# Kernel tuning notes

Hardware: AMD Instinct MI355X
Metric: run time of the kernel (lower is better)

The kernel has to match this reference:

```python
import jax, jax.numpy as jnp
import numpy as np

B, H, C, D = 32, 12, 512, 768
M = 8            # mentions per entity
EMB, BLK = 768, 8
NCLS, NER = 97, 6
OFFSET = 1       # [CLS] offset as in get_hrt


def setup_inputs() -> dict:
    key = jax.random.key(0)
    ks = jax.random.split(key, 10)
    sequence_output = jax.random.normal(ks[0], (B, C, D), jnp.float32)
    attention = jax.random.uniform(ks[1], (B, H, C, C), jnp.float32)
    ner_tags = jax.random.uniform(ks[2], (B, 2, NER), jnp.float32)
    W_head = jax.random.normal(ks[3], (EMB, 2 * D + NER), jnp.float32) * 0.02
    b_head = jnp.zeros((EMB,), jnp.float32)
    W_tail = jax.random.normal(ks[4], (EMB, 2 * D + NER), jnp.float32) * 0.02
    b_tail = jnp.zeros((EMB,), jnp.float32)
    W_bil = jax.random.normal(ks[5], (NCLS, EMB * BLK), jnp.float32) * 0.02
    b_bil = jnp.zeros((NCLS,), jnp.float32)
    entity_pos = jax.random.randint(ks[6], (B, 2, M), 0, C - 2)
    return {"sequence_output": sequence_output, "attention": attention,
            "ner_tags": ner_tags, "W_head": W_head, "b_head": b_head,
            "W_tail": W_tail, "b_tail": b_tail, "W_bil": W_bil,
            "b_bil": b_bil, "entity_pos": entity_pos}


def reference(sequence_output, attention, ner_tags, W_head, b_head,
              W_tail, b_tail, W_bil, b_bil, entity_pos):
    # --- get_hrt, fully vectorized over batch/entities/mentions ---
    pos = entity_pos + OFFSET                       # [B,2,M], all < C
    bidx = jnp.arange(B)[:, None, None]             # [B,1,1]
    # mention embeddings gather + logsumexp over mentions
    ment_emb = sequence_output[bidx, pos]           # [B,2,M,D]
    ent_emb = jax.scipy.special.logsumexp(ment_emb, axis=2)  # [B,2,D]
    # mention attention-row gather + mean over mentions
    att_t = attention.transpose(0, 2, 1, 3)         # [B,C,H,C]
    ment_att = att_t[bidx, pos]                     # [B,2,M,H,C]
    ent_att = ment_att.mean(axis=2)                 # [B,2,H,C]
    # head/tail = entities 0 and 1
    hs = ent_emb[:, 0]                              # [B,D]
    ht_att = (ent_att[:, 0] * ent_att[:, 1]).mean(axis=1)    # [B,C] (mean over heads)
    ht_att = ht_att / (ht_att.sum(axis=1, keepdims=True) + 1e-5)
    rs = jnp.einsum('bld,bl->bd', sequence_output, ht_att)   # [B,D]
    # --- extractors (note: original code concatenates hs in BOTH inputs) ---
    hs_inp = jnp.concatenate([hs, rs, ner_tags[:, 0]], axis=1)  # [B,2D+NER]
    ts_inp = jnp.concatenate([hs, rs, ner_tags[:, 1]], axis=1)  # faithful to source
    hs_f = jnp.tanh(hs_inp @ W_head.T + b_head)     # [B,EMB]
    ts_f = jnp.tanh(ts_inp @ W_tail.T + b_tail)     # [B,EMB]
    # --- grouped bilinear block ---
    b1 = hs_f.reshape(B, EMB // BLK, BLK)
    b2 = ts_f.reshape(B, EMB // BLK, BLK)
    bl = (b1[:, :, :, None] * b2[:, :, None, :]).reshape(B, EMB * BLK)
    logits = bl @ W_bil.T + b_bil                   # [B,NCLS]
    return logits
```

## Files before the change

### kernel.cpp

```cpp
#include <hip/hip_runtime.h>
#include <math.h>

#define BB 32
#define HH 12
#define CC 512
#define DD 768
#define MM 8
#define NERD 6
#define NCLS 97
#define KTOT 1542
#define KMAIN 1536
#define OFFS 1
#define KCH 192
#define APAD 194


__global__ void k_att(const float* __restrict__ att, const float* __restrict__ seq,
                      const int* __restrict__ epos, float* __restrict__ raw,
                      float* __restrict__ Afull) {
    int b = blockIdx.x, h = blockIdx.y;
    __shared__ int pos[16];
    if (threadIdx.x < 16) pos[threadIdx.x] = epos[b * 16 + threadIdx.x] + OFFS;
    __syncthreads();
    if (h < HH) {
        int c = threadIdx.x;
        const float* base = att + ((size_t)(b * HH + h)) * CC * CC;
        float a0 = 0.f, a1 = 0.f;
#pragma unroll
        for (int m = 0; m < MM; m++) {
            a0 += base[(size_t)pos[m] * CC + c];
            a1 += base[(size_t)pos[MM + m] * CC + c];
        }
        atomicAdd(&raw[b * CC + c], a0 * a1 * (1.0f / (MM * MM * HH)));
        return;
    }
    int t = threadIdx.x;
    if (t >= 192) return;
    float xs0[MM], xs1[MM], xs2[MM], xs3[MM];
#pragma unroll
    for (int m = 0; m < MM; m++) {
        float4 v = *(const float4*)&seq[((size_t)b * CC + pos[m]) * DD + t * 4];
        xs0[m] = v.x; xs1[m] = v.y; xs2[m] = v.z; xs3[m] = v.w;
    }
    float o[4];
    float* xs[4] = {xs0, xs1, xs2, xs3};
#pragma unroll
    for (int comp = 0; comp < 4; comp++) {
        float mx = xs[comp][0];
#pragma unroll
        for (int m = 1; m < MM; m++) mx = fmaxf(mx, xs[comp][m]);
        float se = 0.f;
#pragma unroll
        for (int m = 0; m < MM; m++) se += expf(xs[comp][m] - mx);
        o[comp] = logf(se) + mx;
    }
    float4 hv = {o[0], o[1], o[2], o[3]};
    *(float4*)&Afull[(size_t)b * KMAIN + t * 4] = hv;
}

__global__ void k_rs_part(const float* __restrict__ seq, const float* __restrict__ raw,
                          float* __restrict__ rs_part, float* __restrict__ Sb) {
    int b = blockIdx.x, cc = blockIdx.y, t = threadIdx.x;
    float4 acc = {0.f, 0.f, 0.f, 0.f};
    const float* rw = raw + b * CC + cc * 16;
    const float* sp = seq + ((size_t)b * CC + cc * 16) * DD + t * 4;
#pragma unroll 4
    for (int ci = 0; ci < 16; ci++) {
        float w = rw[ci];
        float4 v = *(const float4*)(sp + (size_t)ci * DD);
        acc.x += v.x * w; acc.y += v.y * w; acc.z += v.z * w; acc.w += v.w * w;
    }
    *(float4*)&rs_part[((size_t)(b * 32 + cc)) * DD + t * 4] = acc;
    if (cc == 0) {
        __shared__ float sb[192];
        float s = 0.f;
        for (int c = t; c < CC; c += 192) s += raw[b * CC + c];
        sb[t] = s;
        __syncthreads();
        if (t == 0) {
            float tot = 0.f;
            for (int i = 0; i < 192; i++) tot += sb[i];
            Sb[b] = tot;
        }
    }
}

__global__ void k_rs_fin(const float* __restrict__ rs_part, const float* __restrict__ Sb,
                         float* __restrict__ Afull) {
    int b = blockIdx.x, t = threadIdx.x;
    float4 acc = {0.f, 0.f, 0.f, 0.f};
    for (int cc = 0; cc < 32; cc++) {
        float4 p = *(const float4*)&rs_part[((size_t)(b * 32 + cc)) * DD + t * 4];
        acc.x += p.x; acc.y += p.y; acc.z += p.z; acc.w += p.w;
    }
    float inv = 1.0f / (Sb[b] + 1e-5f);
    float4 r = {acc.x * inv, acc.y * inv, acc.z * inv, acc.w * inv};
    *(float4*)&Afull[(size_t)b * KMAIN + DD + t * 4] = r;
}

__global__ void k_headtail(const float* __restrict__ Afull, const float* __restrict__ ner,
                           const float* __restrict__ Wh, const float* __restrict__ bh,
                           const float* __restrict__ Wt, const float* __restrict__ bt,
                           float* __restrict__ fbuf) {
    int jt = blockIdx.x, e = blockIdx.y;
    int tid = threadIdx.x;
    int b = tid & 31, jq = tid >> 5;
    int j = jt * 8 + jq;
    const float* W = e ? Wt : Wh;
    const float* bias = e ? bt : bh;
    __shared__ float A[32][APAD];
    float acc = 0.f;
    for (int ch = 0; ch < 8; ch++) {
        for (int i = tid; i < 32 * KCH; i += 256) {
            int bb = i / KCH, kk = i - bb * KCH;
            A[bb][kk] = Afull[(size_t)bb * KMAIN + ch * KCH + kk];
        }
        __syncthreads();
        const float* Wrow = W + (size_t)j * KTOT + ch * KCH;
#pragma unroll 8
        for (int kk = 0; kk < KCH; kk += 2) {
            float2 w = *(const float2*)&Wrow[kk];
            float2 a = *(const float2*)&A[b][kk];
            acc += a.x * w.x + a.y * w.y;
        }
        __syncthreads();
    }
    const float* nr = ner + (b * 2 + e) * NERD;
    const float* Wn = W + (size_t)j * KTOT + KMAIN;
#pragma unroll
    for (int q = 0; q < NERD; q++) acc += nr[q] * Wn[q];
    fbuf[(size_t)(e * 32 + b) * DD + j] = tanhf(acc + bias[j]);
}

__global__ void k_bil(const float* __restrict__ fbuf, const float* __restrict__ Wb,
                      const float* __restrict__ bbil, float* __restrict__ out) {
    int n = blockIdx.x;
    int g = threadIdx.x & 7, b = threadIdx.x >> 3;
    const float* hsf = fbuf + b * DD;
    const float* tsf = fbuf + (32 + b) * DD;
    const float* W = Wb + (size_t)n * (DD * 8);
    float acc = 0.f;
    for (int t = 0; t < 12; t++) {
        int f = g + 8 * t;
        float4 h0 = *(const float4*)&hsf[f * 8];
        float4 h1 = *(const float4*)&hsf[f * 8 + 4];
        float4 t0 = *(const float4*)&tsf[f * 8];
        float4 t1 = *(const float4*)&tsf[f * 8 + 4];
        float hv[8] = {h0.x, h0.y, h0.z, h0.w, h1.x, h1.y, h1.z, h1.w};
        float tv[8] = {t0.x, t0.y, t0.z, t0.w, t1.x, t1.y, t1.z, t1.w};
        const float* wf = W + f * 64;
#pragma unroll
        for (int i = 0; i < 8; i++) {
            float4 w0 = *(const float4*)&wf[i * 8];
            float4 w1 = *(const float4*)&wf[i * 8 + 4];
            float dot = tv[0] * w0.x + tv[1] * w0.y + tv[2] * w0.z + tv[3] * w0.w
                      + tv[4] * w1.x + tv[5] * w1.y + tv[6] * w1.z + tv[7] * w1.w;
            acc += hv[i] * dot;
        }
    }
    __shared__ float part[32 * 9];
    part[b * 9 + g] = acc;
    __syncthreads();
    if (g == 0) {
        float s = 0.f;
#pragma unroll
        for (int i = 0; i < 8; i++) s += part[b * 9 + i];
        out[b * NCLS + n] = s + bbil[n];
    }
}

extern "C" void kernel_launch(void* const* d_in, const int* in_sizes, int n_in,
                              void* d_out, int out_size, void* d_ws, size_t ws_size,
                              hipStream_t stream) {
    const float* seq  = (const float*)d_in[0];
    const float* att  = (const float*)d_in[1];
    const float* ner  = (const float*)d_in[2];
    const float* Wh   = (const float*)d_in[3];
    const float* bh   = (const float*)d_in[4];
    const float* Wt   = (const float*)d_in[5];
    const float* bt   = (const float*)d_in[6];
    const float* Wbil = (const float*)d_in[7];
    const float* bbil = (const float*)d_in[8];
    const int*   epos = (const int*)d_in[9];
    float* out = (float*)d_out;
    float* ws = (float*)d_ws;

    float* raw     = ws;
    float* Sb      = ws + 16384;
    float* rs_part = ws + 16416;
    float* Afull   = ws + 802848;
    float* fbuf    = ws + 852000;

    hipMemsetAsync(raw, 0, (size_t)16384 * 4, stream);

    k_att<<<dim3(BB, HH + 1), 512, 0, stream>>>(att, seq, epos, raw, Afull);
    k_rs_part<<<dim3(BB, 32), 192, 0, stream>>>(seq, raw, rs_part, Sb);
    k_rs_fin<<<BB, 192, 0, stream>>>(rs_part, Sb, Afull);
    k_headtail<<<dim3(96, 2), 256, 0, stream>>>(Afull, ner, Wh, bh, Wt, bt, fbuf);
    k_bil<<<NCLS, 256, 0, stream>>>(fbuf, Wbil, bbil, out);
}
```

Baseline: 580.7 us.

## Fuse pipeline into one persistent cooperative kernel with grid syncs

Replaces the memset and five kernel launches with a single cooperative persistent kernel. Its four phases are separated by grid.sync, and a four-kernel fallback path is kept. The attention atomics become per-head partial buffers that are reduced later, the rs partial and finish kernels merge into one phase that accumulates with atomics, and the 1/sum normalisation moves into the head/tail loader. The aim is to cut launch and memset overhead, at the cost of grid-wide barrier latency, fewer resident blocks (512) and float atomics into Afull.

```diff
diff --git a/kernel.cpp b/kernel.cpp
--- a/kernel.cpp
+++ b/kernel.cpp
@@ -1,5 +1,8 @@
 #include <hip/hip_runtime.h>
+#include <hip/hip_cooperative_groups.h>
 #include <math.h>
+
+namespace cg = cooperative_groups;
 
 #define BB 32
 #define HH 12
@@ -13,160 +16,231 @@
 #define OFFS 1
 #define KCH 192
 #define APAD 194
-
-
-__global__ void k_att(const float* __restrict__ att, const float* __restrict__ seq,
-                      const int* __restrict__ epos, float* __restrict__ raw,
-                      float* __restrict__ Afull) {
-    int b = blockIdx.x, h = blockIdx.y;
+#define NTHR 256
+
+
+__device__ __forceinline__ void phaseA(const float* __restrict__ att,
+                                       const float* __restrict__ seq,
+                                       const int* __restrict__ epos,
+                                       float* __restrict__ partial,
+                                       float* __restrict__ Afull,
+                                       float* __restrict__ Sb) {
     __shared__ int pos[16];
-    if (threadIdx.x < 16) pos[threadIdx.x] = epos[b * 16 + threadIdx.x] + OFFS;
-    __syncthreads();
-    if (h < HH) {
-        int c = threadIdx.x;
-        const float* base = att + ((size_t)(b * HH + h)) * CC * CC;
-        float a0 = 0.f, a1 = 0.f;
-#pragma unroll
-        for (int m = 0; m < MM; m++) {
-            a0 += base[(size_t)pos[m] * CC + c];
-            a1 += base[(size_t)pos[MM + m] * CC + c];
-        }
-        atomicAdd(&raw[b * CC + c], a0 * a1 * (1.0f / (MM * MM * HH)));
-        return;
-    }
-    int t = threadIdx.x;
-    if (t >= 192) return;
-    float xs0[MM], xs1[MM], xs2[MM], xs3[MM];
-#pragma unroll
-    for (int m = 0; m < MM; m++) {
-        float4 v = *(const float4*)&seq[((size_t)b * CC + pos[m]) * DD + t * 4];
-        xs0[m] = v.x; xs1[m] = v.y; xs2[m] = v.z; xs3[m] = v.w;
-    }
-    float o[4];
-    float* xs[4] = {xs0, xs1, xs2, xs3};
-#pragma unroll
-    for (int comp = 0; comp < 4; comp++) {
-        float mx = xs[comp][0];
-#pragma unroll
-        for (int m = 1; m < MM; m++) mx = fmaxf(mx, xs[comp][m]);
-        float se = 0.f;
-#pragma unroll
-        for (int m = 0; m < MM; m++) se += expf(xs[comp][m] - mx);
-        o[comp] = logf(se) + mx;
-    }
-    float4 hv = {o[0], o[1], o[2], o[3]};
-    *(float4*)&Afull[(size_t)b * KMAIN + t * 4] = hv;
-}
-
-__global__ void k_rs_part(const float* __restrict__ seq, const float* __restrict__ raw,
-                          float* __restrict__ rs_part, float* __restrict__ Sb) {
-    int b = blockIdx.x, cc = blockIdx.y, t = threadIdx.x;
-    float4 acc = {0.f, 0.f, 0.f, 0.f};
-    const float* rw = raw + b * CC + cc * 16;
-    const float* sp = seq + ((size_t)b * CC + cc * 16) * DD + t * 4;
+    int tid = threadIdx.x;
+    for (int u = blockIdx.x; u < 864; u += gridDim.x) {
+        int b = (u < 768) ? (u / 24) : ((u < 800) ? (u - 768) : (u - 800));
+        __syncthreads();
+        if (tid < 16) pos[tid] = epos[b * 16 + tid] + OFFS;
+        __syncthreads();
+        if (u < 768) {
+            int rem = u - b * 24;
+            int h = rem >> 1, half = rem & 1;
+            int c = half * 256 + tid;
+            const float* base = att + ((size_t)(b * HH + h)) * CC * CC + c;
+            float a0 = 0.f, a1 = 0.f;
+#pragma unroll
+            for (int m = 0; m < MM; m++) {
+                a0 += base[(size_t)pos[m] * CC];
+                a1 += base[(size_t)pos[MM + m] * CC];
+            }
+            partial[((size_t)(b * HH + h)) * CC + c] = a0 * a1 * (1.0f / (MM * MM * HH));
+        } else if (u < 800) {
+            if (tid < 192) {
+                float xs0[MM], xs1[MM], xs2[MM], xs3[MM];
+#pragma unroll
+                for (int m = 0; m < MM; m++) {
+                    float4 v = *(const float4*)&seq[((size_t)b * CC + pos[m]) * DD + tid * 4];
+                    xs0[m] = v.x; xs1[m] = v.y; xs2[m] = v.z; xs3[m] = v.w;
+                }
+                float o[4];
+                float* xs[4] = {xs0, xs1, xs2, xs3};
+#pragma unroll
+                for (int comp = 0; comp < 4; comp++) {
+                    float mx = xs[comp][0];
+#pragma unroll
+                    for (int m = 1; m < MM; m++) mx = fmaxf(mx, xs[comp][m]);
+                    float se = 0.f;
+#pragma unroll
+                    for (int m = 0; m < MM; m++) se += expf(xs[comp][m] - mx);
+                    o[comp] = logf(se) + mx;
+                }
+                float4 hv = {o[0], o[1], o[2], o[3]};
+                *(float4*)&Afull[(size_t)b * KMAIN + tid * 4] = hv;
+            }
+        } else {
+            float* ap = Afull + (size_t)b * KMAIN + DD;
+            ap[tid] = 0.f; ap[tid + 256] = 0.f; ap[tid + 512] = 0.f;
+            if (tid == 0) Sb[b] = 0.f;
+        }
+    }
+}
+
+__device__ __forceinline__ void phaseB(const float* __restrict__ seq,
+                                       const float* __restrict__ partial,
+                                       float* __restrict__ Afull,
+                                       float* __restrict__ Sb) {
+    __shared__ float wsb[16];
+    int tid = threadIdx.x;
+    for (int u = blockIdx.x; u < 1024; u += gridDim.x) {
+        int b = u >> 5, cc = u & 31;
+        int c0 = cc * 16;
+        __syncthreads();
+        if (tid < 16) {
+            float s = 0.f;
+#pragma unroll
+            for (int h = 0; h < HH; h++) s += partial[((size_t)(b * HH + h)) * CC + c0 + tid];
+            wsb[tid] = s;
+        }
+        __syncthreads();
+        if (tid < 192) {
+            float4 acc = {0.f, 0.f, 0.f, 0.f};
+            const float* sp = seq + ((size_t)(b * CC + c0)) * DD + tid * 4;
 #pragma unroll 4
-    for (int ci = 0; ci < 16; ci++) {
-        float w = rw[ci];
-        float4 v = *(const float4*)(sp + (size_t)ci * DD);
-        acc.x += v.x * w; acc.y += v.y * w; acc.z += v.z * w; acc.w += v.w * w;
-    }
-    *(float4*)&rs_part[((size_t)(b * 32 + cc)) * DD + t * 4] = acc;
-    if (cc == 0) {
-        __shared__ float sb[192];
-        float s = 0.f;
-        for (int c = t; c < CC; c += 192) s += raw[b * CC + c];
-        sb[t] = s;
-        __syncthreads();
-        if (t == 0) {
-            float tot = 0.f;
-            for (int i = 0; i < 192; i++) tot += sb[i];
-            Sb[b] = tot;
-        }
-    }
-}
-
-__global__ void k_rs_fin(const float* __restrict__ rs_part, const float* __restrict__ Sb,
-                         float* __restrict__ Afull) {
-    int b = blockIdx.x, t = threadIdx.x;
-    float4 acc = {0.f, 0.f, 0.f, 0.f};
-    for (int cc = 0; cc < 32; cc++) {
-        float4 p = *(const float4*)&rs_part[((size_t)(b * 32 + cc)) * DD + t * 4];
-        acc.x += p.x; acc.y += p.y; acc.z += p.z; acc.w += p.w;
-    }
-    float inv = 1.0f / (Sb[b] + 1e-5f);
-    float4 r = {acc.x * inv, acc.y * inv, acc.z * inv, acc.w * inv};
-    *(float4*)&Afull[(size_t)b * KMAIN + DD + t * 4] = r;
-}
-
-__global__ void k_headtail(const float* __restrict__ Afull, const float* __restrict__ ner,
-                           const float* __restrict__ Wh, const float* __restrict__ bh,
-                           const float* __restrict__ Wt, const float* __restrict__ bt,
-                           float* __restrict__ fbuf) {
-    int jt = blockIdx.x, e = blockIdx.y;
-    int tid = threadIdx.x;
-    int b = tid & 31, jq = tid >> 5;
-    int j = jt * 8 + jq;
-    const float* W = e ? Wt : Wh;
-    const float* bias = e ? bt : bh;
-    __shared__ float A[32][APAD];
-    float acc = 0.f;
-    for (int ch = 0; ch < 8; ch++) {
-        for (int i = tid; i < 32 * KCH; i += 256) {
-            int bb = i / KCH, kk = i - bb * KCH;
-            A[bb][kk] = Afull[(size_t)bb * KMAIN + ch * KCH + kk];
-        }
-        __syncthreads();
-        const float* Wrow = W + (size_t)j * KTOT + ch * KCH;
+            for (int ci = 0; ci < 16; ci++) {
+                float w = wsb[ci];
+                float4 v = *(const float4*)(sp + (size_t)ci * DD);
+                acc.x += v.x * w; acc.y += v.y * w; acc.z += v.z * w; acc.w += v.w * w;
+            }
+            float* ap = &Afull[(size_t)b * KMAIN + DD + tid * 4];
+            atomicAdd(ap + 0, acc.x); atomicAdd(ap + 1, acc.y);
+            atomicAdd(ap + 2, acc.z); atomicAdd(ap + 3, acc.w);
+        }
+        if (tid == 0) {
+            float s = 0.f;
+#pragma unroll
+            for (int i = 0; i < 16; i++) s += wsb[i];
+            atomicAdd(&Sb[b], s);
+        }
+    }
+}
+
+__device__ __forceinline__ void phaseC(const float* __restrict__ Afull,
+                                       const float* __restrict__ Sb,
+                                       const float* __restrict__ ner,
+                                       const float* __restrict__ Wh,
+                                       const float* __restrict__ bh,
+                                       const float* __restrict__ Wt,
+                                       const float* __restrict__ bt,
+                                       float* __restrict__ fbuf) {
+    __shared__ float invS[BB];
+    __shared__ float A[BB][APAD];
+    int tid = threadIdx.x;
+    for (int u = blockIdx.x; u < 192; u += gridDim.x) {
+        int jt = u >> 1, e = u & 1;
+        __syncthreads();
+        if (tid < BB) invS[tid] = 1.0f / (Sb[tid] + 1e-5f);
+        __syncthreads();
+        int b = tid & 31, jq = tid >> 5;
+        int j = jt * 8 + jq;
+        const float* W = e ? Wt : Wh;
+        float acc = 0.f;
+        for (int ch = 0; ch < 8; ch++) {
+            for (int i = tid; i < 32 * KCH; i += NTHR) {
+                int bb = i / KCH, kk = i - bb * KCH;
+                int k = ch * KCH + kk;
+                float v = Afull[(size_t)bb * KMAIN + k];
+                if (k >= DD) v *= invS[bb];
+                A[bb][kk] = v;
+            }
+            __syncthreads();
+            const float* Wrow = W + (size_t)j * KTOT + ch * KCH;
 #pragma unroll 8
-        for (int kk = 0; kk < KCH; kk += 2) {
-            float2 w = *(const float2*)&Wrow[kk];
-            float2 a = *(const float2*)&A[b][kk];
-            acc += a.x * w.x + a.y * w.y;
-        }
-        __syncthreads();
-    }
-    const float* nr = ner + (b * 2 + e) * NERD;
-    const float* Wn = W + (size_t)j * KTOT + KMAIN;
-#pragma unroll
-    for (int q = 0; q < NERD; q++) acc += nr[q] * Wn[q];
-    fbuf[(size_t)(e * 32 + b) * DD + j] = tanhf(acc + bias[j]);
-}
-
-__global__ void k_bil(const float* __restrict__ fbuf, const float* __restrict__ Wb,
-                      const float* __restrict__ bbil, float* __restrict__ out) {
-    int n = blockIdx.x;
-    int g = threadIdx.x & 7, b = threadIdx.x >> 3;
-    const float* hsf = fbuf + b * DD;
-    const float* tsf = fbuf + (32 + b) * DD;
-    const float* W = Wb + (size_t)n * (DD * 8);
-    float acc = 0.f;
-    for (int t = 0; t < 12; t++) {
-        int f = g + 8 * t;
-        float4 h0 = *(const float4*)&hsf[f * 8];
-        float4 h1 = *(const float4*)&hsf[f * 8 + 4];
-        float4 t0 = *(const float4*)&tsf[f * 8];
-        float4 t1 = *(const float4*)&tsf[f * 8 + 4];
-        float hv[8] = {h0.x, h0.y, h0.z, h0.w, h1.x, h1.y, h1.z, h1.w};
-        float tv[8] = {t0.x, t0.y, t0.z, t0.w, t1.x, t1.y, t1.z, t1.w};
-        const float* wf = W + f * 64;
-#pragma unroll
-        for (int i = 0; i < 8; i++) {
-            float4 w0 = *(const float4*)&wf[i * 8];
-            float4 w1 = *(const float4*)&wf[i * 8 + 4];
-            float dot = tv[0] * w0.x + tv[1] * w0.y + tv[2] * w0.z + tv[3] * w0.w
-                      + tv[4] * w1.x + tv[5] * w1.y + tv[6] * w1.z + tv[7] * w1.w;
-            acc += hv[i] * dot;
-        }
-    }
-    __shared__ float part[32 * 9];
-    part[b * 9 + g] = acc;
-    __syncthreads();
-    if (g == 0) {
-        float s = 0.f;
-#pragma unroll
-        for (int i = 0; i < 8; i++) s += part[b * 9 + i];
-        out[b * NCLS + n] = s + bbil[n];
-    }
+            for (int kk = 0; kk < KCH; kk += 2) {
+                float2 w = *(const float2*)&Wrow[kk];
+                float2 a = *(const float2*)&A[b][kk];
+                acc += a.x * w.x + a.y * w.y;
+            }
+            __syncthreads();
+        }
+        const float* nr = ner + (b * 2 + e) * NERD;
+        const float* Wn = W + (size_t)j * KTOT + KMAIN;
+#pragma unroll
+        for (int q = 0; q < NERD; q++) acc += nr[q] * Wn[q];
+        const float* bias = e ? bt : bh;
+        fbuf[(size_t)(e * 32 + b) * DD + j] = tanhf(acc + bias[j]);
+    }
+}
+
+__device__ __forceinline__ void phaseD(const float* __restrict__ fbuf,
+                                       const float* __restrict__ Wbil,
+                                       const float* __restrict__ bbil,
+                                       float* __restrict__ out) {
+    __shared__ float part[BB * 9];
+    int tid = threadIdx.x;
+    for (int n = blockIdx.x; n < NCLS; n += gridDim.x) {
+        __syncthreads();
+        int g = tid & 7, b = tid >> 3;
+        const float* hsf = fbuf + b * DD;
+        const float* tsf = fbuf + (32 + b) * DD;
+        const float* W = Wbil + (size_t)n * (DD * 8);
+        float acc = 0.f;
+        for (int t = 0; t < 12; t++) {
+            int f = g + 8 * t;
+            float4 h0 = *(const float4*)&hsf[f * 8];
+            float4 h1 = *(const float4*)&hsf[f * 8 + 4];
+            float4 t0 = *(const float4*)&tsf[f * 8];
+            float4 t1 = *(const float4*)&tsf[f * 8 + 4];
+            float hv[8] = {h0.x, h0.y, h0.z, h0.w, h1.x, h1.y, h1.z, h1.w};
+            float tv[8] = {t0.x, t0.y, t0.z, t0.w, t1.x, t1.y, t1.z, t1.w};
+            const float* wf = W + f * 64;
+#pragma unroll
+            for (int i = 0; i < 8; i++) {
+                float4 w0 = *(const float4*)&wf[i * 8];
+                float4 w1 = *(const float4*)&wf[i * 8 + 4];
+                float dot = tv[0] * w0.x + tv[1] * w0.y + tv[2] * w0.z + tv[3] * w0.w
+                          + tv[4] * w1.x + tv[5] * w1.y + tv[6] * w1.z + tv[7] * w1.w;
+                acc += hv[i] * dot;
+            }
+        }
+        part[b * 9 + g] = acc;
+        __syncthreads();
+        if (g == 0) {
+            float s = 0.f;
+#pragma unroll
+            for (int i = 0; i < 8; i++) s += part[b * 9 + i];
+            out[b * NCLS + n] = s + bbil[n];
+        }
+    }
+}
+
+__global__ void __launch_bounds__(NTHR, 2) k_fused(
+    const float* __restrict__ seq, const float* __restrict__ att,
+    const float* __restrict__ ner,
+    const float* __restrict__ Wh, const float* __restrict__ bh,
+    const float* __restrict__ Wt, const float* __restrict__ bt,
+    const float* __restrict__ Wbil, const float* __restrict__ bbil,
+    const int* __restrict__ epos,
+    float* __restrict__ partial, float* __restrict__ Afull,
+    float* __restrict__ Sb, float* __restrict__ fbuf,
+    float* __restrict__ out) {
+    cg::grid_group grid = cg::this_grid();
+    phaseA(att, seq, epos, partial, Afull, Sb);
+    grid.sync();
+    phaseB(seq, partial, Afull, Sb);
+    grid.sync();
+    phaseC(Afull, Sb, ner, Wh, bh, Wt, bt, fbuf);
+    grid.sync();
+    phaseD(fbuf, Wbil, bbil, out);
+}
+
+__global__ void __launch_bounds__(NTHR) kA(const float* att, const float* seq,
+                                           const int* epos, float* partial,
+                                           float* Afull, float* Sb) {
+    phaseA(att, seq, epos, partial, Afull, Sb);
+}
+__global__ void __launch_bounds__(NTHR) kB(const float* seq, const float* partial,
+                                           float* Afull, float* Sb) {
+    phaseB(seq, partial, Afull, Sb);
+}
+__global__ void __launch_bounds__(NTHR) kC(const float* Afull, const float* Sb,
+                                           const float* ner, const float* Wh,
+                                           const float* bh, const float* Wt,
+                                           const float* bt, float* fbuf) {
+    phaseC(Afull, Sb, ner, Wh, bh, Wt, bt, fbuf);
+}
+__global__ void __launch_bounds__(NTHR) kD(const float* fbuf, const float* Wbil,
+                                           const float* bbil, float* out) {
+    phaseD(fbuf, Wbil, bbil, out);
 }
 
 extern "C" void kernel_launch(void* const* d_in, const int* in_sizes, int n_in,
@@ -185,17 +259,27 @@
     float* out = (float*)d_out;
     float* ws = (float*)d_ws;
 
-    float* raw     = ws;
-    float* Sb      = ws + 16384;
-    float* rs_part = ws + 16416;
-    float* Afull   = ws + 802848;
-    float* fbuf    = ws + 852000;
-
-    hipMemsetAsync(raw, 0, (size_t)16384 * 4, stream);
-
-    k_att<<<dim3(BB, HH + 1), 512, 0, stream>>>(att, seq, epos, raw, Afull);
-    k_rs_part<<<dim3(BB, 32), 192, 0, stream>>>(seq, raw, rs_part, Sb);
-    k_rs_fin<<<BB, 192, 0, stream>>>(rs_part, Sb, Afull);
-    k_headtail<<<dim3(96, 2), 256, 0, stream>>>(Afull, ner, Wh, bh, Wt, bt, fbuf);
-    k_bil<<<NCLS, 256, 0, stream>>>(fbuf, Wbil, bbil, out);
-}
+    float* partial = ws;
+    float* Afull   = ws + 196608;
+    float* Sb      = ws + 245760;
+    float* fbuf    = ws + 245792;
+
+    int mb = 0;
+    hipOccupancyMaxActiveBlocksPerMultiprocessor(&mb, k_fused, NTHR, 0);
+    bool coop_ok = false;
+    if (mb >= 1) {
+        int bpc = mb > 2 ? 2 : mb;
+        dim3 grid(256 * bpc);
+        void* args[] = {(void*)&seq, (void*)&att, (void*)&ner, (void*)&Wh, (void*)&bh,
+                        (void*)&Wt, (void*)&bt, (void*)&Wbil, (void*)&bbil, (void*)&epos,
+                        (void*)&partial, (void*)&Afull, (void*)&Sb, (void*)&fbuf, (void*)&out};
+        coop_ok = (hipLaunchCooperativeKernel(k_fused, grid, dim3(NTHR), args, 0, stream)
+                   == hipSuccess);
+    }
+    if (!coop_ok) {
+        kA<<<864, NTHR, 0, stream>>>(att, seq, epos, partial, Afull, Sb);
+        kB<<<1024, NTHR, 0, stream>>>(seq, partial, Afull, Sb);
+        kC<<<192, NTHR, 0, stream>>>(Afull, Sb, ner, Wh, bh, Wt, bt, fbuf);
+        kD<<<97, NTHR, 0, stream>>>(fbuf, Wbil, bbil, out);
+    }
+}
```

New measurement: 804.4 us. 1.39x slower.
